# Optimization experiments

Hardware: AMD Instinct MI355X
Metric: run time of the kernel (lower is better)

The kernel has to match this reference:

```python
import jax, jax.numpy as jnp
import numpy as np

N_NODES = 100000

def _sage_conv(x, src, dst, w_l, b_l, w_r):
    # PyG SAGEConv (mean aggr): out = lin_l(mean_j x_j) + lin_r(x_i)
    msg = x[src]                                             # [E, d] gather
    agg = jax.ops.segment_sum(msg, dst, num_segments=N_NODES)
    deg = jax.ops.segment_sum(jnp.ones((src.shape[0],), x.dtype), dst,
                              num_segments=N_NODES)
    mean = agg / jnp.maximum(deg, 1.0)[:, None]
    return mean @ w_l.T + b_l + x @ w_r.T


def setup_inputs() -> dict:
    key = jax.random.key(0)
    ks = jax.random.split(key, 9)
    d_in, d_h, d_out = 128, 128, 4
    E = 1600000
    x = jax.random.normal(ks[0], (N_NODES, d_in), dtype=jnp.float32)
    edge_index = jax.random.randint(ks[1], (2, E), 0, N_NODES, dtype=jnp.int32)
    s = lambda k, shp, fan: jax.random.normal(k, shp, jnp.float32) / np.sqrt(fan)
    return {
        "x": x,
        "edge_index": edge_index,
        "w1_l": s(ks[2], (d_h, d_in), d_in),
        "b1_l": jnp.zeros((d_h,), jnp.float32),
        "w1_r": s(ks[3], (d_h, d_in), d_in),
        "w2_l": s(ks[4], (d_h, d_h), d_h),
        "b2_l": jnp.zeros((d_h,), jnp.float32),
        "w2_r": s(ks[5], (d_h, d_h), d_h),
        "w_out": s(ks[6], (d_out, d_h), d_h),
        "b_out": jnp.zeros((d_out,), jnp.float32),
    }


def reference(x, edge_index, w1_l, b1_l, w1_r, w2_l, b2_l, w2_r, w_out, b_out):
    src, dst = edge_index[0], edge_index[1]
    h = jax.nn.relu(_sage_conv(x, src, dst, w1_l, b1_l, w1_r))
    h = jax.nn.relu(_sage_conv(h, src, dst, w2_l, b2_l, w2_r))
    return h @ w_out.T + b_out
```

## Files before the change

### kernel.cpp

```cpp
#include <hip/hip_runtime.h>

constexpr int D = 128;
constexpr int BSHIFT = 9;
constexpr int BNODES = 1 << BSHIFT;
constexpr int NBUCK_MAX = 256;
using short8 = __attribute__((ext_vector_type(8))) short;
using f32x4  = __attribute__((ext_vector_type(4))) float;

__device__ __forceinline__ unsigned rneb(float f) {
    unsigned u = __float_as_uint(f);
    return (u + 0x7fffu + ((u >> 16) & 1u)) >> 16;
}
__device__ __forceinline__ float lo2f(unsigned u) { return __uint_as_float(u << 16); }
__device__ __forceinline__ float hi2f(unsigned u) { return __uint_as_float(u & 0xffff0000u); }

__global__ __launch_bounds__(256) void f32_to_bf16(
    const float* __restrict__ in, unsigned short* __restrict__ out, int n4)
{
    int i = blockIdx.x * 256 + threadIdx.x;
    if (i >= n4) return;
    float4 v = reinterpret_cast<const float4*>(in)[i];
    uint2 o;
    o.x = rneb(v.x) | (rneb(v.y) << 16);
    o.y = rneb(v.z) | (rneb(v.w) << 16);
    reinterpret_cast<uint2*>(out)[i] = o;
}

__global__ __launch_bounds__(256) void pack_w(
    const float* __restrict__ w1l, const float* __restrict__ w1r,
    const float* __restrict__ w2l, const float* __restrict__ w2r,
    unsigned short* __restrict__ wf)
{
    int t = blockIdx.x * 256 + threadIdx.x;
    int m = t >> 11;
    int r = t & 2047;
    int f = r >> 6, lane = r & 63;
    int c = f >> 2, ks = f & 3;
    int col = c * 16 + (lane & 15);
    int k0 = ks * 32 + (lane >> 4) * 8;
    const float* W = (m == 0) ? w1l : (m == 1) ? w1r : (m == 2) ? w2l : w2r;
    unsigned short o[8];
#pragma unroll
    for (int i = 0; i < 8; ++i) o[i] = (unsigned short)rneb(W[col * D + k0 + i]);
    uint4 pk;
    pk.x = o[0] | ((unsigned)o[1] << 16);
    pk.y = o[2] | ((unsigned)o[3] << 16);
    pk.z = o[4] | ((unsigned)o[5] << 16);
    pk.w = o[6] | ((unsigned)o[7] << 16);
    reinterpret_cast<uint4*>(wf)[t] = pk;
}

__global__ __launch_bounds__(256) void bucket_count(
    const int* __restrict__ dstI, int* __restrict__ bcnt, int E, int nb)
{
    __shared__ int lh[NBUCK_MAX];
    const int t = threadIdx.x;
    const int e0 = blockIdx.x * 4096;
    for (int i = t; i < nb; i += 256) lh[i] = 0;
    __syncthreads();
#pragma unroll
    for (int q = 0; q < 16; ++q) {
        int e = e0 + q * 256 + t;
        if (e < E) atomicAdd(&lh[dstI[e] >> BSHIFT], 1);
    }
    __syncthreads();
    for (int b = t; b < nb; b += 256)
        if (lh[b] > 0) atomicAdd(&bcnt[b], lh[b]);
}

__global__ __launch_bounds__(256) void bucket_scan(
    const int* __restrict__ bcnt, int* __restrict__ bbase,
    int* __restrict__ gcursor, int nb)
{
    __shared__ int tmp[256];
    const int t = threadIdx.x;
    const int v = (t < nb) ? bcnt[t] : 0;
    tmp[t] = v;
    __syncthreads();
    for (int off = 1; off < 256; off <<= 1) {
        int u = (t >= off) ? tmp[t - off] : 0;
        __syncthreads();
        tmp[t] += u;
        __syncthreads();
    }
    int excl = tmp[t] - v;
    if (t < nb) { bbase[t] = excl; gcursor[t] = excl; }
    if (t == nb - 1) bbase[nb] = excl + v;
}

__global__ __launch_bounds__(256) void bin_kernel(
    const int* __restrict__ srcI, const int* __restrict__ dstI,
    int* __restrict__ gcursor, unsigned* __restrict__ binned, int E, int nb)
{
    __shared__ int lhist[NBUCK_MAX];
    __shared__ int lbase[NBUCK_MAX];
    __shared__ int lcnt[NBUCK_MAX];
    const int t = threadIdx.x;
    const int e0 = blockIdx.x * 4096;
    for (int i = t; i < nb; i += 256) { lhist[i] = 0; lcnt[i] = 0; }
    __syncthreads();

    int dcache[16], scache[16];
#pragma unroll
    for (int q = 0; q < 16; ++q) {
        int e = e0 + q * 256 + t;
        int d = (e < E) ? dstI[e] : -1;
        dcache[q] = d;
        scache[q] = (e < E) ? srcI[e] : 0;
        if (d >= 0) atomicAdd(&lhist[d >> BSHIFT], 1);
    }
    __syncthreads();
    for (int b = t; b < nb; b += 256)
        if (lhist[b] > 0) lbase[b] = atomicAdd(&gcursor[b], lhist[b]);
    __syncthreads();
#pragma unroll
    for (int q = 0; q < 16; ++q) {
        int d = dcache[q];
        if (d >= 0) {
            int b = d >> BSHIFT;
            int off = atomicAdd(&lcnt[b], 1);
            binned[lbase[b] + off] =
                (unsigned)scache[q] | ((unsigned)(d & (BNODES - 1)) << 17);
        }
    }
}

__global__ __launch_bounds__(256) void bucket_build(
    const unsigned* __restrict__ binned, const int* __restrict__ bbase,
    int* __restrict__ rowptr, int* __restrict__ sorted_src, int n, int E)
{
    __shared__ int hist[BNODES];
    __shared__ int cur[BNODES];
    __shared__ int tmp[256];
    const int t = threadIdx.x;
    const int b = blockIdx.x;
    const int node0 = b << BSHIFT;
    const int ebeg = bbase[b];
    const int eend = bbase[b + 1];

    hist[t] = 0; hist[t + 256] = 0;
    __syncthreads();
    for (int e = ebeg + t; e < eend; e += 256)
        atomicAdd(&hist[(binned[e] >> 17) & (BNODES - 1)], 1);
    __syncthreads();

    const int v0 = hist[2 * t], v1 = hist[2 * t + 1];
    const int s = v0 + v1;
    tmp[t] = s;
    __syncthreads();
    for (int off = 1; off < 256; off <<= 1) {
        int u = (t >= off) ? tmp[t - off] : 0;
        __syncthreads();
        tmp[t] += u;
        __syncthreads();
    }
    const int pre = ebeg + tmp[t] - s;
    const int i0 = node0 + 2 * t, i1 = i0 + 1;
    cur[2 * t] = pre;
    cur[2 * t + 1] = pre + v0;
    if (i0 < n) rowptr[i0] = pre;
    if (i1 < n) rowptr[i1] = pre + v0;
    if (b == 0 && t == 0) rowptr[n] = E;
    __syncthreads();

    for (int e = ebeg + t; e < eend; e += 256) {
        unsigned w = binned[e];
        int pos = atomicAdd(&cur[(w >> 17) & (BNODES - 1)], 1);
        sorted_src[pos] = (int)(w & 0x1FFFF);
    }
}

__global__ __launch_bounds__(256) void aggregate_bf16(
    const unsigned short* __restrict__ feat, const int* __restrict__ sorted_src,
    const int* __restrict__ rowptr, unsigned short* __restrict__ outb, int n)
{
    const int wid = (blockIdx.x * 256 + threadIdx.x) >> 6;
    if (wid >= n) return;
    const int lane = threadIdx.x & 63;
    const int sub = lane >> 4;
    const int part = lane & 15;
    const int beg = rowptr[wid];
    const int end = rowptr[wid + 1];
    const int deg = end - beg;

    float acc[8];
#pragma unroll
    for (int j = 0; j < 8; ++j) acc[j] = 0.f;

    int e = beg;
    for (; e + 8 <= end; e += 8) {
        const int s0 = sorted_src[e + sub];
        const int s1 = sorted_src[e + 4 + sub];
        const uint4 v0 = *reinterpret_cast<const uint4*>(feat + (size_t)s0 * D + part * 8);
        const uint4 v1 = *reinterpret_cast<const uint4*>(feat + (size_t)s1 * D + part * 8);
        acc[0] += lo2f(v0.x); acc[1] += hi2f(v0.x);
        acc[2] += lo2f(v0.y); acc[3] += hi2f(v0.y);
        acc[4] += lo2f(v0.z); acc[5] += hi2f(v0.z);
        acc[6] += lo2f(v0.w); acc[7] += hi2f(v0.w);
        acc[0] += lo2f(v1.x); acc[1] += hi2f(v1.x);
        acc[2] += lo2f(v1.y); acc[3] += hi2f(v1.y);
        acc[4] += lo2f(v1.z); acc[5] += hi2f(v1.z);
        acc[6] += lo2f(v1.w); acc[7] += hi2f(v1.w);
    }
    if (e + 4 <= end) {
        const int s0 = sorted_src[e + sub];
        const uint4 v0 = *reinterpret_cast<const uint4*>(feat + (size_t)s0 * D + part * 8);
        acc[0] += lo2f(v0.x); acc[1] += hi2f(v0.x);
        acc[2] += lo2f(v0.y); acc[3] += hi2f(v0.y);
        acc[4] += lo2f(v0.z); acc[5] += hi2f(v0.z);
        acc[6] += lo2f(v0.w); acc[7] += hi2f(v0.w);
        e += 4;
    }
    if (e < end) {
        const int ei = e + sub;
        const bool act = ei < end;
        const int s = act ? sorted_src[ei] : sorted_src[beg];
        const float m = act ? 1.f : 0.f;
        const uint4 v = *reinterpret_cast<const uint4*>(feat + (size_t)s * D + part * 8);
        acc[0] += m * lo2f(v.x); acc[1] += m * hi2f(v.x);
        acc[2] += m * lo2f(v.y); acc[3] += m * hi2f(v.y);
        acc[4] += m * lo2f(v.z); acc[5] += m * hi2f(v.z);
        acc[6] += m * lo2f(v.w); acc[7] += m * hi2f(v.w);
    }

#pragma unroll
    for (int j = 0; j < 8; ++j) {
        acc[j] += __shfl_xor(acc[j], 16);
        acc[j] += __shfl_xor(acc[j], 32);
    }

    if (sub == 0) {
        const float inv = (deg > 0) ? 1.0f / (float)deg : 0.f;
        uint4 pk;
        pk.x = rneb(acc[0] * inv) | (rneb(acc[1] * inv) << 16);
        pk.y = rneb(acc[2] * inv) | (rneb(acc[3] * inv) << 16);
        pk.z = rneb(acc[4] * inv) | (rneb(acc[5] * inv) << 16);
        pk.w = rneb(acc[6] * inv) | (rneb(acc[7] * inv) << 16);
        *reinterpret_cast<uint4*>(outb + (size_t)wid * D + part * 8) = pk;
    }
}

__global__ __launch_bounds__(256) void mfma_gemm(
    const unsigned short* __restrict__ aMean, const unsigned short* __restrict__ aSelf,
    const unsigned short* __restrict__ wfL, const unsigned short* __restrict__ wfR,
    const float* __restrict__ bL, unsigned short* __restrict__ outb, int n)
{
    const int lane = threadIdx.x & 63;
    const int wave = threadIdx.x >> 6;
    const int lo = lane & 15, hi = lane >> 4;
    const int row0 = blockIdx.x * 64 + wave * 16;
    int arow = row0 + lo;
    if (arow > n - 1) arow = n - 1;
    const size_t abase = (size_t)arow * D;

    f32x4 acc[8];
#pragma unroll
    for (int c = 0; c < 8; ++c) acc[c] = (f32x4){0.f, 0.f, 0.f, 0.f};

#pragma unroll
    for (int p = 0; p < 2; ++p) {
        const unsigned short* A  = p ? aSelf : aMean;
        const unsigned short* WF = p ? wfR : wfL;
#pragma unroll
        for (int ks = 0; ks < 4; ++ks) {
            short8 af = *reinterpret_cast<const short8*>(A + abase + ks * 32 + hi * 8);
#pragma unroll
            for (int c = 0; c < 8; ++c) {
                short8 bf = *reinterpret_cast<const short8*>(
                    WF + ((((c << 2) | ks) * 64 + lane) << 3));
                acc[c] = __builtin_amdgcn_mfma_f32_16x16x32_bf16(af, bf, acc[c], 0, 0, 0);
            }
        }
    }

#pragma unroll
    for (int c = 0; c < 8; ++c) {
        const int col = (c << 4) | lo;
        const float bias = bL[col];
#pragma unroll
        for (int j = 0; j < 4; ++j) {
            const int row = row0 + (hi << 2) + j;
            if (row < n)
                outb[(size_t)row * D + col] =
                    (unsigned short)rneb(fmaxf(acc[c][j] + bias, 0.f));
        }
    }
}

__global__ __launch_bounds__(256) void mfma_gemm_out(
    const unsigned short* __restrict__ aMean, const unsigned short* __restrict__ aSelf,
    const unsigned short* __restrict__ wfL, const unsigned short* __restrict__ wfR,
    const float* __restrict__ bL, const float* __restrict__ w_out,
    const float* __restrict__ b_out, float* __restrict__ outp, int n)
{
    __shared__ float wsm[4 * D];
    wsm[threadIdx.x] = w_out[threadIdx.x];
    wsm[threadIdx.x + 256] = w_out[threadIdx.x + 256];
    __syncthreads();

    const int lane = threadIdx.x & 63;
    const int wave = threadIdx.x >> 6;
    const int lo = lane & 15, hi = lane >> 4;
    const int row0 = blockIdx.x * 64 + wave * 16;
    int arow = row0 + lo;
    if (arow > n - 1) arow = n - 1;
    const size_t abase = (size_t)arow * D;

    f32x4 acc[8];
#pragma unroll
    for (int c = 0; c < 8; ++c) acc[c] = (f32x4){0.f, 0.f, 0.f, 0.f};

#pragma unroll
    for (int p = 0; p < 2; ++p) {
        const unsigned short* A  = p ? aSelf : aMean;
        const unsigned short* WF = p ? wfR : wfL;
#pragma unroll
        for (int ks = 0; ks < 4; ++ks) {
            short8 af = *reinterpret_cast<const short8*>(A + abase + ks * 32 + hi * 8);
#pragma unroll
            for (int c = 0; c < 8; ++c) {
                short8 bf = *reinterpret_cast<const short8*>(
                    WF + ((((c << 2) | ks) * 64 + lane) << 3));
                acc[c] = __builtin_amdgcn_mfma_f32_16x16x32_bf16(af, bf, acc[c], 0, 0, 0);
            }
        }
    }

    float part[4][4];
#pragma unroll
    for (int j = 0; j < 4; ++j)
#pragma unroll
        for (int d = 0; d < 4; ++d) part[j][d] = 0.f;

#pragma unroll
    for (int c = 0; c < 8; ++c) {
        const int col = (c << 4) | lo;
        const float bias = bL[col];
        const float w0 = wsm[0 * D + col];
        const float w1 = wsm[1 * D + col];
        const float w2 = wsm[2 * D + col];
        const float w3 = wsm[3 * D + col];
#pragma unroll
        for (int j = 0; j < 4; ++j) {
            const float h = fmaxf(acc[c][j] + bias, 0.f);
            part[j][0] += h * w0;
            part[j][1] += h * w1;
            part[j][2] += h * w2;
            part[j][3] += h * w3;
        }
    }

#pragma unroll
    for (int m = 1; m < 16; m <<= 1) {
#pragma unroll
        for (int j = 0; j < 4; ++j)
#pragma unroll
            for (int d = 0; d < 4; ++d)
                part[j][d] += __shfl_xor(part[j][d], m);
    }

    if (lo == 0) {
        const float4 bo = *reinterpret_cast<const float4*>(b_out);
#pragma unroll
        for (int j = 0; j < 4; ++j) {
            const int row = row0 + (hi << 2) + j;
            if (row < n) {
                float4 o;
                o.x = part[j][0] + bo.x;
                o.y = part[j][1] + bo.y;
                o.z = part[j][2] + bo.z;
                o.w = part[j][3] + bo.w;
                *reinterpret_cast<float4*>(outp + (size_t)row * 4) = o;
            }
        }
    }
}

extern "C" void kernel_launch(void* const* d_in, const int* in_sizes, int n_in,
                              void* d_out, int out_size, void* d_ws, size_t ws_size,
                              hipStream_t stream)
{
    const float* x    = (const float*)d_in[0];
    const int*   ei   = (const int*)  d_in[1];
    const float* w1l  = (const float*)d_in[2];
    const float* b1l  = (const float*)d_in[3];
    const float* w1r  = (const float*)d_in[4];
    const float* w2l  = (const float*)d_in[5];
    const float* b2l  = (const float*)d_in[6];
    const float* w2r  = (const float*)d_in[7];
    const float* wout = (const float*)d_in[8];
    const float* bout = (const float*)d_in[9];

    const int n = in_sizes[0] / D;
    const int E = in_sizes[1] / 2;
    const int* srcI = ei;
    const int* dstI = ei + E;
    const int nbuck = (n + BNODES - 1) >> BSHIFT;

    auto align256 = [](size_t v) { return (v + 255) & ~(size_t)255; };
    char* base = (char*)d_ws;
    size_t off = 0;
    int* bcnt = (int*)(base + off);            off = align256(off + sizeof(int) * NBUCK_MAX);
    int* bbase = (int*)(base + off);           off = align256(off + sizeof(int) * (NBUCK_MAX + 1));
    int* gcursor = (int*)(base + off);         off = align256(off + sizeof(int) * NBUCK_MAX);
    int* rowptr = (int*)(base + off);          off = align256(off + sizeof(int) * (size_t)(n + 1));
    int* sorted_src = (int*)(base + off);      off = align256(off + sizeof(int) * (size_t)E);
    unsigned* binned = (unsigned*)(base + off); off = align256(off + sizeof(unsigned) * (size_t)E);
    unsigned short* xb = (unsigned short*)(base + off);
    off = align256(off + sizeof(short) * (size_t)n * D);
    unsigned short* bufA = (unsigned short*)(base + off);
    off = align256(off + sizeof(short) * (size_t)n * D);
    unsigned short* bufB = (unsigned short*)(base + off);
    off = align256(off + sizeof(short) * (size_t)n * D);
    unsigned short* wf = (unsigned short*)(base + off);

    hipMemsetAsync(bcnt, 0, sizeof(int) * NBUCK_MAX, stream);
    const int ebblocks = (E + 4095) / 4096;
    bucket_count<<<ebblocks, 256, 0, stream>>>(dstI, bcnt, E, nbuck);
    bucket_scan<<<1, 256, 0, stream>>>(bcnt, bbase, gcursor, nbuck);
    bin_kernel<<<ebblocks, 256, 0, stream>>>(srcI, dstI, gcursor, binned, E, nbuck);
    bucket_build<<<nbuck, 256, 0, stream>>>(binned, bbase, rowptr, sorted_src, n, E);

    pack_w<<<32, 256, 0, stream>>>(w1l, w1r, w2l, w2r, wf);
    const int n4 = n * (D / 4);
    f32_to_bf16<<<(n4 + 255) / 256, 256, 0, stream>>>(x, xb, n4);

    const int ablocks = (int)(((long long)n * 64 + 255) / 256);
    const int gblocks = (n + 63) / 64;

    aggregate_bf16<<<ablocks, 256, 0, stream>>>(xb, sorted_src, rowptr, bufA, n);
    mfma_gemm<<<gblocks, 256, 0, stream>>>(bufA, xb, wf, wf + 16384, b1l, bufA, n);

    aggregate_bf16<<<ablocks, 256, 0, stream>>>(bufA, sorted_src, rowptr, bufB, n);
    mfma_gemm_out<<<gblocks, 256, 0, stream>>>(bufB, bufA, wf + 2 * 16384, wf + 3 * 16384,
                                               b2l, wout, bout, (float*)d_out, n);
}
```

Measured before the change: 356.7 us.

## Fuse setup kernels with last-block scan; split aggregation columns across block pairs

Weight packing, the x-to-bf16 conversion, bucket counting and the bucket scan are merged into one launch. The last counting block, found through an atomic done counter and thread fences, performs the scan, which removes three kernel launches and their serialization. The aggregation kernel now gives each half of the 128 feature columns to a separate block, so every wave handles 8 edges per step at 64 columns. This doubles the edge parallelism per node at the cost of twice as many index loads and one more shuffle-reduction step.

Result: slower. 406.3 us (+13.9%).

```diff
diff --git a/kernel.cpp b/kernel.cpp
--- a/kernel.cpp
+++ b/kernel.cpp
@@ -14,48 +14,51 @@
 __device__ __forceinline__ float lo2f(unsigned u) { return __uint_as_float(u << 16); }
 __device__ __forceinline__ float hi2f(unsigned u) { return __uint_as_float(u & 0xffff0000u); }
 
-__global__ __launch_bounds__(256) void f32_to_bf16(
-    const float* __restrict__ in, unsigned short* __restrict__ out, int n4)
-{
-    int i = blockIdx.x * 256 + threadIdx.x;
-    if (i >= n4) return;
-    float4 v = reinterpret_cast<const float4*>(in)[i];
-    uint2 o;
-    o.x = rneb(v.x) | (rneb(v.y) << 16);
-    o.y = rneb(v.z) | (rneb(v.w) << 16);
-    reinterpret_cast<uint2*>(out)[i] = o;
-}
-
-__global__ __launch_bounds__(256) void pack_w(
+__global__ __launch_bounds__(256) void misc_count_kernel(
     const float* __restrict__ w1l, const float* __restrict__ w1r,
     const float* __restrict__ w2l, const float* __restrict__ w2r,
-    unsigned short* __restrict__ wf)
-{
-    int t = blockIdx.x * 256 + threadIdx.x;
-    int m = t >> 11;
-    int r = t & 2047;
-    int f = r >> 6, lane = r & 63;
-    int c = f >> 2, ks = f & 3;
-    int col = c * 16 + (lane & 15);
-    int k0 = ks * 32 + (lane >> 4) * 8;
-    const float* W = (m == 0) ? w1l : (m == 1) ? w1r : (m == 2) ? w2l : w2r;
-    unsigned short o[8];
-#pragma unroll
-    for (int i = 0; i < 8; ++i) o[i] = (unsigned short)rneb(W[col * D + k0 + i]);
-    uint4 pk;
-    pk.x = o[0] | ((unsigned)o[1] << 16);
-    pk.y = o[2] | ((unsigned)o[3] << 16);
-    pk.z = o[4] | ((unsigned)o[5] << 16);
-    pk.w = o[6] | ((unsigned)o[7] << 16);
-    reinterpret_cast<uint4*>(wf)[t] = pk;
-}
-
-__global__ __launch_bounds__(256) void bucket_count(
-    const int* __restrict__ dstI, int* __restrict__ bcnt, int E, int nb)
-{
+    unsigned short* __restrict__ wf,
+    const float* __restrict__ x, unsigned short* __restrict__ xb, int n4,
+    const int* __restrict__ dstI, int* __restrict__ bcnt, int* __restrict__ done,
+    int* __restrict__ bbase, int* __restrict__ gcursor,
+    int E, int nb, int cvtblocks, int countblocks)
+{
+    const int t = threadIdx.x;
+    if (blockIdx.x < 32) {
+        int g = blockIdx.x * 256 + t;
+        int m = g >> 11;
+        int r = g & 2047;
+        int f = r >> 6, lane = r & 63;
+        int c = f >> 2, ks = f & 3;
+        int col = c * 16 + (lane & 15);
+        int k0 = ks * 32 + (lane >> 4) * 8;
+        const float* W = (m == 0) ? w1l : (m == 1) ? w1r : (m == 2) ? w2l : w2r;
+        unsigned short o[8];
+#pragma unroll
+        for (int i = 0; i < 8; ++i) o[i] = (unsigned short)rneb(W[col * D + k0 + i]);
+        uint4 pk;
+        pk.x = o[0] | ((unsigned)o[1] << 16);
+        pk.y = o[2] | ((unsigned)o[3] << 16);
+        pk.z = o[4] | ((unsigned)o[5] << 16);
+        pk.w = o[6] | ((unsigned)o[7] << 16);
+        reinterpret_cast<uint4*>(wf)[g] = pk;
+        return;
+    }
+    if (blockIdx.x < 32 + cvtblocks) {
+        int i = (blockIdx.x - 32) * 256 + t;
+        if (i >= n4) return;
+        float4 v = reinterpret_cast<const float4*>(x)[i];
+        uint2 o;
+        o.x = rneb(v.x) | (rneb(v.y) << 16);
+        o.y = rneb(v.z) | (rneb(v.w) << 16);
+        reinterpret_cast<uint2*>(xb)[i] = o;
+        return;
+    }
+
     __shared__ int lh[NBUCK_MAX];
-    const int t = threadIdx.x;
-    const int e0 = blockIdx.x * 4096;
+    __shared__ int isLast;
+    const int cb = blockIdx.x - 32 - cvtblocks;
+    const int e0 = cb * 4096;
     for (int i = t; i < nb; i += 256) lh[i] = 0;
     __syncthreads();
 #pragma unroll
@@ -66,24 +69,24 @@
     __syncthreads();
     for (int b = t; b < nb; b += 256)
         if (lh[b] > 0) atomicAdd(&bcnt[b], lh[b]);
-}
-
-__global__ __launch_bounds__(256) void bucket_scan(
-    const int* __restrict__ bcnt, int* __restrict__ bbase,
-    int* __restrict__ gcursor, int nb)
-{
-    __shared__ int tmp[256];
-    const int t = threadIdx.x;
-    const int v = (t < nb) ? bcnt[t] : 0;
-    tmp[t] = v;
+    __threadfence();
+    if (t == 0) {
+        int old = atomicAdd(done, 1);
+        isLast = (old == countblocks - 1) ? 1 : 0;
+    }
+    __syncthreads();
+    if (!isLast) return;
+    __threadfence();
+    const int v = (t < nb) ? atomicAdd(&bcnt[t], 0) : 0;
+    lh[t] = v;
     __syncthreads();
     for (int off = 1; off < 256; off <<= 1) {
-        int u = (t >= off) ? tmp[t - off] : 0;
+        int u = (t >= off) ? lh[t - off] : 0;
         __syncthreads();
-        tmp[t] += u;
+        lh[t] += u;
         __syncthreads();
     }
-    int excl = tmp[t] - v;
+    int excl = lh[t] - v;
     if (t < nb) { bbase[t] = excl; gcursor[t] = excl; }
     if (t == nb - 1) bbase[nb] = excl + v;
 }
@@ -174,11 +177,13 @@
     const unsigned short* __restrict__ feat, const int* __restrict__ sorted_src,
     const int* __restrict__ rowptr, unsigned short* __restrict__ outb, int n)
 {
-    const int wid = (blockIdx.x * 256 + threadIdx.x) >> 6;
+    const int half = blockIdx.x & 1;
+    const int wid = (((blockIdx.x >> 1) * 256) + threadIdx.x) >> 6;
     if (wid >= n) return;
     const int lane = threadIdx.x & 63;
-    const int sub = lane >> 4;
-    const int part = lane & 15;
+    const int sub = lane >> 3;
+    const int part = lane & 7;
+    const int colb = half * 64 + part * 8;
     const int beg = rowptr[wid];
     const int end = rowptr[wid + 1];
     const int deg = end - beg;
@@ -188,11 +193,11 @@
     for (int j = 0; j < 8; ++j) acc[j] = 0.f;
 
     int e = beg;
-    for (; e + 8 <= end; e += 8) {
+    for (; e + 16 <= end; e += 16) {
         const int s0 = sorted_src[e + sub];
-        const int s1 = sorted_src[e + 4 + sub];
-        const uint4 v0 = *reinterpret_cast<const uint4*>(feat + (size_t)s0 * D + part * 8);
-        const uint4 v1 = *reinterpret_cast<const uint4*>(feat + (size_t)s1 * D + part * 8);
+        const int s1 = sorted_src[e + 8 + sub];
+        const uint4 v0 = *reinterpret_cast<const uint4*>(feat + (size_t)s0 * D + colb);
+        const uint4 v1 = *reinterpret_cast<const uint4*>(feat + (size_t)s1 * D + colb);
         acc[0] += lo2f(v0.x); acc[1] += hi2f(v0.x);
         acc[2] += lo2f(v0.y); acc[3] += hi2f(v0.y);
         acc[4] += lo2f(v0.z); acc[5] += hi2f(v0.z);
@@ -202,21 +207,21 @@
         acc[4] += lo2f(v1.z); acc[5] += hi2f(v1.z);
         acc[6] += lo2f(v1.w); acc[7] += hi2f(v1.w);
     }
-    if (e + 4 <= end) {
+    if (e + 8 <= end) {
         const int s0 = sorted_src[e + sub];
-        const uint4 v0 = *reinterpret_cast<const uint4*>(feat + (size_t)s0 * D + part * 8);
+        const uint4 v0 = *reinterpret_cast<const uint4*>(feat + (size_t)s0 * D + colb);
         acc[0] += lo2f(v0.x); acc[1] += hi2f(v0.x);
         acc[2] += lo2f(v0.y); acc[3] += hi2f(v0.y);
         acc[4] += lo2f(v0.z); acc[5] += hi2f(v0.z);
         acc[6] += lo2f(v0.w); acc[7] += hi2f(v0.w);
-        e += 4;
+        e += 8;
     }
     if (e < end) {
         const int ei = e + sub;
         const bool act = ei < end;
         const int s = act ? sorted_src[ei] : sorted_src[beg];
         const float m = act ? 1.f : 0.f;
-        const uint4 v = *reinterpret_cast<const uint4*>(feat + (size_t)s * D + part * 8);
+        const uint4 v = *reinterpret_cast<const uint4*>(feat + (size_t)s * D + colb);
         acc[0] += m * lo2f(v.x); acc[1] += m * hi2f(v.x);
         acc[2] += m * lo2f(v.y); acc[3] += m * hi2f(v.y);
         acc[4] += m * lo2f(v.z); acc[5] += m * hi2f(v.z);
@@ -225,6 +230,7 @@
 
 #pragma unroll
     for (int j = 0; j < 8; ++j) {
+        acc[j] += __shfl_xor(acc[j], 8);
         acc[j] += __shfl_xor(acc[j], 16);
         acc[j] += __shfl_xor(acc[j], 32);
     }
@@ -236,7 +242,7 @@
         pk.y = rneb(acc[2] * inv) | (rneb(acc[3] * inv) << 16);
         pk.z = rneb(acc[4] * inv) | (rneb(acc[5] * inv) << 16);
         pk.w = rneb(acc[6] * inv) | (rneb(acc[7] * inv) << 16);
-        *reinterpret_cast<uint4*>(outb + (size_t)wid * D + part * 8) = pk;
+        *reinterpret_cast<uint4*>(outb + (size_t)wid * D + colb) = pk;
     }
 }
 
@@ -400,7 +406,8 @@
     auto align256 = [](size_t v) { return (v + 255) & ~(size_t)255; };
     char* base = (char*)d_ws;
     size_t off = 0;
-    int* bcnt = (int*)(base + off);            off = align256(off + sizeof(int) * NBUCK_MAX);
+    int* bcnt = (int*)(base + off);            off = align256(off + sizeof(int) * (NBUCK_MAX + 1));
+    int* done = bcnt + NBUCK_MAX;
     int* bbase = (int*)(base + off);           off = align256(off + sizeof(int) * (NBUCK_MAX + 1));
     int* gcursor = (int*)(base + off);         off = align256(off + sizeof(int) * NBUCK_MAX);
     int* rowptr = (int*)(base + off);          off = align256(off + sizeof(int) * (size_t)(n + 1));
@@ -414,18 +421,19 @@
     off = align256(off + sizeof(short) * (size_t)n * D);
     unsigned short* wf = (unsigned short*)(base + off);
 
-    hipMemsetAsync(bcnt, 0, sizeof(int) * NBUCK_MAX, stream);
+    hipMemsetAsync(bcnt, 0, sizeof(int) * (NBUCK_MAX + 1), stream);
+    const int n4 = n * (D / 4);
+    const int cvtblocks = (n4 + 255) / 256;
     const int ebblocks = (E + 4095) / 4096;
-    bucket_count<<<ebblocks, 256, 0, stream>>>(dstI, bcnt, E, nbuck);
-    bucket_scan<<<1, 256, 0, stream>>>(bcnt, bbase, gcursor, nbuck);
+    misc_count_kernel<<<32 + cvtblocks + ebblocks, 256, 0, stream>>>(
+        w1l, w1r, w2l, w2r, wf, x, xb, n4,
+        dstI, bcnt, done, bbase, gcursor, E, nbuck, cvtblocks, ebblocks);
+
     bin_kernel<<<ebblocks, 256, 0, stream>>>(srcI, dstI, gcursor, binned, E, nbuck);
     bucket_build<<<nbuck, 256, 0, stream>>>(binned, bbase, rowptr, sorted_src, n, E);
 
-    pack_w<<<32, 256, 0, stream>>>(w1l, w1r, w2l, w2r, wf);
-    const int n4 = n * (D / 4);
-    f32_to_bf16<<<(n4 + 255) / 256, 256, 0, stream>>>(x, xb, n4);
-
-    const int ablocks = (int)(((long long)n * 64 + 255) / 256);
+    const int nodeblocks = (n + 3) / 4;
+    const int ablocks = nodeblocks * 2;
     const int gblocks = (n + 63) / 64;
 
     aggregate_bf16<<<ablocks, 256, 0, stream>>>(xb, sorted_src, rowptr, bufA, n);
```
